# Optimization experiments

Measured on AMD Instinct MI355X. Metric: run time of the kernel, lower is better.

Reference implementation:

```python
import jax, jax.numpy as jnp
import numpy as np

B = 4096          # effective_batch_size (world_size=1)
D = 128           # embedding_dim
T = 0.5           # temperature
CW = 0.5          # confidence_weight
PT = 0.8          # positive_threshold (cosine)


def setup_inputs() -> dict:
    key = jax.random.key(0)
    emb = jax.random.normal(key, (B, D), dtype=jnp.float32)
    emb = emb / jnp.linalg.norm(emb, axis=1, keepdims=True)  # cosine-sim embeddings
    return {"embedding": emb}


def reference(embedding):
    b = embedding.shape[0]
    half = b // 2
    idx = jnp.arange(b)
    pos_idx = (idx + half) % b  # positive pair index (other augmented view)

    # exp(sim / T), [B, B]
    sim = jnp.exp(embedding @ embedding.T / T)

    # precomputed masks (world_size=1, rank=0, num_pos=2):
    # positive mask: the other view; negative mask: everything except self and its pair
    pos_mask = jnp.zeros((b, b), dtype=sim.dtype).at[idx, pos_idx].set(1.0)
    neg_mask = 1.0 - pos_mask - jnp.eye(b, dtype=sim.dtype)

    all_pos = sim * pos_mask
    all_neg = sim * neg_mask

    pos_sim = sim[idx, pos_idx]  # [B]

    # diff_sim: |sim - pos_sim| on upper triangle (j >= i), 3 elsewhere,
    # with diagonal and (i, i+half) for i < half also set to 3
    upper = idx[None, :] >= idx[:, None]
    excl = jnp.eye(b, dtype=bool) | ((idx[:, None] < half) & (idx[None, :] == idx[:, None] + half))
    diff_sim = jnp.where(upper & ~excl, jnp.abs(sim - pos_sim[:, None]), jnp.asarray(3.0, sim.dtype))

    # all argmin locations (torch.where(diff_sim == min)) -> boolean select mask
    min_mask = diff_sim == jnp.min(diff_sim)
    conf = (jnp.log(pos_sim) * T >= PT)[:, None]  # per-anchor confidence gate
    sel = min_mask & conf

    # false-negative reweighting (pos read of all_neg happens before neg update)
    new_pos = jnp.where(sel & (all_pos == 0.0), CW * all_neg, all_pos)
    new_neg = jnp.where(sel & (all_neg != 0.0), (1.0 - CW) * all_neg, all_neg)

    pos = jnp.sum(new_pos, axis=1)
    neg = jnp.sum(new_neg, axis=1)
    return -jnp.mean(jnp.log(pos / (pos + neg)))
```

## Files before the change

### kernel.cpp

```cpp
#include <hip/hip_runtime.h>
#include <hip/hip_bf16.h>
#include <math.h>

#define B_N  4096
#define HALF 2048
#define D_K  128
#define BT   128
#define NBT  32
#define NBLK (NBT * (NBT + 1) / 2)

typedef __attribute__((ext_vector_type(8))) short bf16x8;
typedef __attribute__((ext_vector_type(4))) float f32x4;

__device__ __forceinline__ void stage_tile_cvt(const float* __restrict__ emb,
                                               int row0, ushort* lds) {
    int t = threadIdx.x;
    const float4* src = (const float4*)(emb + (size_t)row0 * D_K);
    char* dst = (char*)lds;
#pragma unroll
    for (int it = 0; it < 8; ++it) {
        int f = t + 256 * it;
        int r = f >> 4;
        int c = f & 15;
        float4 v0 = src[r * 32 + c * 2];
        float4 v1 = src[r * 32 + c * 2 + 1];
        union { __hip_bfloat162 h; unsigned u; } c0, c1, c2, c3;
        c0.h = __float22bfloat162_rn(make_float2(v0.x, v0.y));
        c1.h = __float22bfloat162_rn(make_float2(v0.z, v0.w));
        c2.h = __float22bfloat162_rn(make_float2(v1.x, v1.y));
        c3.h = __float22bfloat162_rn(make_float2(v1.z, v1.w));
        uint4 w = {c0.u, c1.u, c2.u, c3.u};
        int byte = (r << 8) | (((c ^ (r & 7)) & 15) << 4);
        *(uint4*)(dst + byte) = w;
    }
}

__device__ __forceinline__ bf16x8 read_frag(const ushort* lds, int row, int kbyte) {
    int byte = ((row << 8) | kbyte) ^ ((row & 7) << 4);
    return *(const bf16x8*)((const char*)lds + byte);
}

__device__ __forceinline__ void tile_mfma_sw(const ushort* Al, const ushort* Bl,
                                             int lane, int wr, f32x4 acc[2][8]) {
#pragma unroll
    for (int m = 0; m < 2; ++m)
#pragma unroll
        for (int n = 0; n < 8; ++n) acc[m][n] = (f32x4){0.f, 0.f, 0.f, 0.f};

    int rA = wr * 32 + (lane & 15);
    int rB = (lane & 15);
    int kb0 = (lane >> 4) << 4;
#pragma unroll
    for (int ks = 0; ks < 4; ++ks) {
        int kb = ks * 64 + kb0;
        bf16x8 a[2], b[8];
#pragma unroll
        for (int m = 0; m < 2; ++m) a[m] = read_frag(Al, rA + m * 16, kb);
#pragma unroll
        for (int n = 0; n < 8; ++n) b[n] = read_frag(Bl, rB + n * 16, kb);
#pragma unroll
        for (int m = 0; m < 2; ++m)
#pragma unroll
            for (int n = 0; n < 8; ++n)
                acc[m][n] = __builtin_amdgcn_mfma_f32_16x16x32_bf16(
                    b[n], a[m], acc[m][n], 0, 0, 0);
    }
}

__global__ __launch_bounds__(256) void k0_prep(const float* __restrict__ emb,
                                               float* __restrict__ pos_sim,
                                               float* __restrict__ conf,
                                               float* __restrict__ neg_acc,
                                               unsigned* __restrict__ minbits,
                                               unsigned* __restrict__ counter) {
    int tid = threadIdx.x;
    int r   = blockIdx.x * 16 + (tid >> 4);
    int l16 = tid & 15;
    const float* a = emb + (size_t)r * D_K + l16 * 8;
    const float* b = emb + (size_t)(r ^ HALF) * D_K + l16 * 8;
    float4 x0 = *(const float4*)a,       x1 = *(const float4*)(a + 4);
    float4 y0 = *(const float4*)b,       y1 = *(const float4*)(b + 4);
    float d = 0.f;
    d = fmaf(x0.x, y0.x, d); d = fmaf(x0.y, y0.y, d);
    d = fmaf(x0.z, y0.z, d); d = fmaf(x0.w, y0.w, d);
    d = fmaf(x1.x, y1.x, d); d = fmaf(x1.y, y1.y, d);
    d = fmaf(x1.z, y1.z, d); d = fmaf(x1.w, y1.w, d);
#pragma unroll
    for (int off = 1; off < 16; off <<= 1) d += __shfl_xor(d, off);
    if (l16 == 0) {
        float ps = expf(d * 2.0f);
        pos_sim[r] = ps;
        conf[r]    = (logf(ps) * 0.5f >= 0.8f) ? 1.0f : 0.0f;
        neg_acc[r] = 0.f;
    }
    if (blockIdx.x == 0 && tid == 0) {
        *minbits = __float_as_uint(3.0f);
        *counter = 0u;
    }
}

__global__ __launch_bounds__(256, 2) void k1_main(const float* __restrict__ emb,
                                                  const float* __restrict__ pos_sim,
                                                  const float* __restrict__ conf,
                                                  float* __restrict__ neg_acc,
                                                  float* __restrict__ corrpart,
                                                  unsigned* __restrict__ block_min,
                                                  unsigned* __restrict__ minbits) {
    int t = blockIdx.x, bi = 0;
    while (t >= NBT - bi) { t -= NBT - bi; ++bi; }
    int bj = bi + t;
    bool diag = (bi == bj);
    bool post = (bj == (bi ^ 16));

    __shared__ ushort Al[BT * D_K];
    __shared__ ushort Bl[BT * D_K];
    stage_tile_cvt(emb, bi * BT, Al);
    if (!diag) stage_tile_cvt(emb, bj * BT, Bl);
    __syncthreads();
    const ushort* Bs = diag ? Al : Bl;

    int tid = threadIdx.x, lane = tid & 63, wr = tid >> 6;
    f32x4 acc[2][8];
    tile_mfma_sw(Al, Bs, lane, wr, acc);

#pragma unroll
    for (int m = 0; m < 2; ++m)
#pragma unroll
        for (int n = 0; n < 8; ++n)
#pragma unroll
            for (int reg = 0; reg < 4; ++reg)
                acc[m][n][reg] = __expf(acc[m][n][reg] * 2.0f);

    int ib = bi * BT + wr * 32 + (lane & 15);
    int jb = bj * BT + ((lane >> 4) << 2);

    float psi_[2];
    float lmin = 3.0f;
#pragma unroll
    for (int m = 0; m < 2; ++m) {
        int i = ib + m * 16;
        float psi = pos_sim[i];
        psi_[m] = psi;
        int pidx = i ^ HALF;
        float np0 = 0.f, np1 = 0.f, np2 = 0.f, np3 = 0.f;
        float l0 = 3.f, l1 = 3.f, l2 = 3.f, l3 = 3.f;
        if (!diag && !post) {
#pragma unroll
            for (int n = 0; n < 8; ++n) {
                float s0 = acc[m][n][0], s1 = acc[m][n][1];
                float s2 = acc[m][n][2], s3 = acc[m][n][3];
                np0 += s0; np1 += s1; np2 += s2; np3 += s3;
                l0 = fminf(l0, fabsf(s0 - psi)); l1 = fminf(l1, fabsf(s1 - psi));
                l2 = fminf(l2, fabsf(s2 - psi)); l3 = fminf(l3, fabsf(s3 - psi));
            }
        } else if (diag) {
#pragma unroll
            for (int n = 0; n < 8; ++n)
#pragma unroll
                for (int reg = 0; reg < 4; ++reg) {
                    float s = acc[m][n][reg];
                    int j = jb + n * 16 + reg;
                    if (j != i) np0 += s;
                    if (j > i)  l0 = fminf(l0, fabsf(s - psi));
                }
        } else {
#pragma unroll
            for (int n = 0; n < 8; ++n)
#pragma unroll
                for (int reg = 0; reg < 4; ++reg) {
                    float s = acc[m][n][reg];
                    int j = jb + n * 16 + reg;
                    if (j != pidx) {
                        np0 += s;
                        l0 = fminf(l0, fabsf(s - psi));
                    }
                }
        }
        float negp = (np0 + np1) + (np2 + np3);
        negp += __shfl_xor(negp, 16);
        negp += __shfl_xor(negp, 32);
        if (lane < 16) atomicAdd(&neg_acc[i], negp);
        lmin = fminf(lmin, fminf(fminf(l0, l1), fminf(l2, l3)));
    }

    if (!diag) {
        float colc[32];
#pragma unroll
        for (int n = 0; n < 8; ++n)
#pragma unroll
            for (int reg = 0; reg < 4; ++reg) {
                float s0 = acc[0][n][reg], s1 = acc[1][n][reg];
                if (post) {
                    int j = jb + n * 16 + reg;
                    if (j == (ib ^ HALF))        s0 = 0.f;
                    if (j == ((ib + 16) ^ HALF)) s1 = 0.f;
                }
                colc[n * 4 + reg] = s0 + s1;
            }
#pragma unroll
        for (int off = 1; off < 16; off <<= 1)
#pragma unroll
            for (int v = 0; v < 32; ++v)
                colc[v] += __shfl_xor(colc[v], off);
        if ((lane & 15) == 0) {
#pragma unroll
            for (int v = 0; v < 32; ++v)
                atomicAdd(&neg_acc[jb + (v >> 2) * 16 + (v & 3)], colc[v]);
        }
    }

#pragma unroll
    for (int off = 32; off; off >>= 1)
        lmin = fminf(lmin, __shfl_xor(lmin, off));
    __shared__ float wred[4];
    if (lane == 0) wred[wr] = lmin;
    __syncthreads();
    float bmin = fminf(fminf(wred[0], wred[1]), fminf(wred[2], wred[3]));
    if (tid == 0) {
        block_min[bi * NBT + bj] = __float_as_uint(bmin);
        atomicMin(minbits, __float_as_uint(bmin));
    }

    float corr_[2] = {0.f, 0.f};
    bool anyc = (conf[ib] != 0.f) || (conf[ib + 16] != 0.f);
    if (__any(anyc)) {
#pragma unroll
        for (int m = 0; m < 2; ++m) {
            int i = ib + m * 16;
            float psi = psi_[m];
            int pidx = i ^ HALF;
            bool ci = (conf[i] != 0.f);
            float corr = 0.f;
#pragma unroll
            for (int n = 0; n < 8; ++n)
#pragma unroll
                for (int reg = 0; reg < 4; ++reg) {
                    float s = acc[m][n][reg];
                    int j = jb + n * 16 + reg;
                    bool valid = diag ? (j > i) : (post ? (j != pidx) : true);
                    float d = valid ? fabsf(s - psi) : 3.0f;
                    if (ci && d == bmin) corr += 0.5f * s;
                }
            corr += __shfl_xor(corr, 16);
            corr += __shfl_xor(corr, 32);
            corr_[m] = corr;
        }
    }
    if (lane < 16) {
        corrpart[bj * B_N + ib]      = corr_[0];
        corrpart[bj * B_N + ib + 16] = corr_[1];
    }
}

__global__ __launch_bounds__(128) void k3_loss(const float* __restrict__ pos_sim,
                                               const float* __restrict__ neg_acc,
                                               const float* __restrict__ corrpart,
                                               const unsigned* __restrict__ block_min,
                                               const unsigned* __restrict__ minbits,
                                               float* __restrict__ partial,
                                               unsigned* __restrict__ counter,
                                               float* __restrict__ out) {
    int bi = blockIdx.x, t = threadIdx.x;
    int i = bi * 128 + t;
    unsigned gm = *minbits;
    float corr = 0.f;
    for (int bj = bi; bj < NBT; ++bj)
        if (block_min[bi * NBT + bj] == gm) corr += corrpart[bj * B_N + i];
    float neg = neg_acc[i] - corr;
    float pos = pos_sim[i] + corr;
    float l = logf(pos / (pos + neg));
#pragma unroll
    for (int off = 32; off; off >>= 1) l += __shfl_xor(l, off);
    __shared__ float w2[2];
    if ((t & 63) == 0) w2[t >> 6] = l;
    __syncthreads();
    if (t == 0) {
        partial[bi] = w2[0] + w2[1];
        __threadfence();
        unsigned c = atomicAdd((unsigned*)counter, 1u);
        if (c == NBT - 1) {
            __threadfence();
            float tot = 0.f;
            volatile float* vp = partial;
            for (int b = 0; b < NBT; ++b) tot += vp[b];
            *out = -tot / (float)B_N;
        }
    }
}

extern "C" void kernel_launch(void* const* d_in, const int* in_sizes, int n_in,
                              void* d_out, int out_size, void* d_ws, size_t ws_size,
                              hipStream_t stream) {
    const float* emb = (const float*)d_in[0];
    float* out = (float*)d_out;

    float* fbase = (float*)d_ws;
    float*    pos_sim   = fbase;
    float*    conf      = fbase + 4096;
    float*    neg_acc   = fbase + 8192;
    float*    corrpart  = fbase + 12288;
    float*    partial   = corrpart + NBT * B_N;
    unsigned* block_min = (unsigned*)(partial + 32);
    unsigned* minbits   = block_min + 1024;
    unsigned* counter   = minbits + 1;

    k0_prep<<<256, 256, 0, stream>>>(emb, pos_sim, conf, neg_acc, minbits, counter);
    k1_main<<<NBLK, 256, 0, stream>>>(emb, pos_sim, conf, neg_acc, corrpart,
                                      block_min, minbits);
    k3_loss<<<NBT, 128, 0, stream>>>(pos_sim, neg_acc, corrpart, block_min,
                                     minbits, partial, counter, out);
}
```

Baseline: 40.59 us.

## Precompute bf16 embeddings and stream full-row j-tiles with async LDS double buffering

```diff
diff --git a/kernel.cpp b/kernel.cpp
--- a/kernel.cpp
+++ b/kernel.cpp
@@ -5,34 +5,26 @@
 #define B_N  4096
 #define HALF 2048
 #define D_K  128
-#define BT   128
-#define NBT  32
-#define NBLK (NBT * (NBT + 1) / 2)
+#define TI   128
+#define TJ   64
+#define NTI  32
+#define NTJ  64
+#define JPB  4
+#define NJG  (NTJ / JPB)
 
 typedef __attribute__((ext_vector_type(8))) short bf16x8;
 typedef __attribute__((ext_vector_type(4))) float f32x4;
 
-__device__ __forceinline__ void stage_tile_cvt(const float* __restrict__ emb,
-                                               int row0, ushort* lds) {
-    int t = threadIdx.x;
-    const float4* src = (const float4*)(emb + (size_t)row0 * D_K);
-    char* dst = (char*)lds;
-#pragma unroll
-    for (int it = 0; it < 8; ++it) {
-        int f = t + 256 * it;
-        int r = f >> 4;
-        int c = f & 15;
-        float4 v0 = src[r * 32 + c * 2];
-        float4 v1 = src[r * 32 + c * 2 + 1];
-        union { __hip_bfloat162 h; unsigned u; } c0, c1, c2, c3;
-        c0.h = __float22bfloat162_rn(make_float2(v0.x, v0.y));
-        c1.h = __float22bfloat162_rn(make_float2(v0.z, v0.w));
-        c2.h = __float22bfloat162_rn(make_float2(v1.x, v1.y));
-        c3.h = __float22bfloat162_rn(make_float2(v1.z, v1.w));
-        uint4 w = {c0.u, c1.u, c2.u, c3.u};
-        int byte = (r << 8) | (((c ^ (r & 7)) & 15) << 4);
-        *(uint4*)(dst + byte) = w;
-    }
+__device__ __forceinline__ ushort f2bf(float x) {
+    unsigned u = __float_as_uint(x);
+    unsigned r = u + 0x7FFFu + ((u >> 16) & 1u);
+    return (ushort)(r >> 16);
+}
+
+__device__ __forceinline__ void gload_lds16(const ushort* g, ushort* l) {
+    __builtin_amdgcn_global_load_lds(
+        (const __attribute__((address_space(1))) unsigned int*)g,
+        (__attribute__((address_space(3))) unsigned int*)l, 16, 0, 0);
 }
 
 __device__ __forceinline__ bf16x8 read_frag(const ushort* lds, int row, int kbyte) {
@@ -40,234 +32,258 @@
     return *(const bf16x8*)((const char*)lds + byte);
 }
 
-__device__ __forceinline__ void tile_mfma_sw(const ushort* Al, const ushort* Bl,
-                                             int lane, int wr, f32x4 acc[2][8]) {
-#pragma unroll
-    for (int m = 0; m < 2; ++m)
-#pragma unroll
-        for (int n = 0; n < 8; ++n) acc[m][n] = (f32x4){0.f, 0.f, 0.f, 0.f};
-
-    int rA = wr * 32 + (lane & 15);
-    int rB = (lane & 15);
-    int kb0 = (lane >> 4) << 4;
-#pragma unroll
-    for (int ks = 0; ks < 4; ++ks) {
-        int kb = ks * 64 + kb0;
-        bf16x8 a[2], b[8];
-#pragma unroll
-        for (int m = 0; m < 2; ++m) a[m] = read_frag(Al, rA + m * 16, kb);
-#pragma unroll
-        for (int n = 0; n < 8; ++n) b[n] = read_frag(Bl, rB + n * 16, kb);
-#pragma unroll
-        for (int m = 0; m < 2; ++m)
-#pragma unroll
-            for (int n = 0; n < 8; ++n)
-                acc[m][n] = __builtin_amdgcn_mfma_f32_16x16x32_bf16(
-                    b[n], a[m], acc[m][n], 0, 0, 0);
-    }
-}
-
 __global__ __launch_bounds__(256) void k0_prep(const float* __restrict__ emb,
+                                               ushort* __restrict__ embh,
                                                float* __restrict__ pos_sim,
                                                float* __restrict__ conf,
                                                float* __restrict__ neg_acc,
-                                               unsigned* __restrict__ minbits,
+                                               float* __restrict__ corrpart,
                                                unsigned* __restrict__ counter) {
     int tid = threadIdx.x;
-    int r   = blockIdx.x * 16 + (tid >> 4);
-    int l16 = tid & 15;
-    const float* a = emb + (size_t)r * D_K + l16 * 8;
-    const float* b = emb + (size_t)(r ^ HALF) * D_K + l16 * 8;
-    float4 x0 = *(const float4*)a,       x1 = *(const float4*)(a + 4);
-    float4 y0 = *(const float4*)b,       y1 = *(const float4*)(b + 4);
-    float d = 0.f;
-    d = fmaf(x0.x, y0.x, d); d = fmaf(x0.y, y0.y, d);
-    d = fmaf(x0.z, y0.z, d); d = fmaf(x0.w, y0.w, d);
-    d = fmaf(x1.x, y1.x, d); d = fmaf(x1.y, y1.y, d);
-    d = fmaf(x1.z, y1.z, d); d = fmaf(x1.w, y1.w, d);
-#pragma unroll
-    for (int off = 1; off < 16; off <<= 1) d += __shfl_xor(d, off);
-    if (l16 == 0) {
-        float ps = expf(d * 2.0f);
-        pos_sim[r] = ps;
-        conf[r]    = (logf(ps) * 0.5f >= 0.8f) ? 1.0f : 0.0f;
-        neg_acc[r] = 0.f;
-    }
-    if (blockIdx.x == 0 && tid == 0) {
-        *minbits = __float_as_uint(3.0f);
-        *counter = 0u;
-    }
-}
-
-__global__ __launch_bounds__(256, 2) void k1_main(const float* __restrict__ emb,
+    int gtid = blockIdx.x * 256 + tid;
+    float4 v = ((const float4*)emb)[gtid];
+    ushort4 h;
+    h.x = f2bf(v.x); h.y = f2bf(v.y); h.z = f2bf(v.z); h.w = f2bf(v.w);
+    ((ushort4*)embh)[gtid] = h;
+    ((float2*)corrpart)[gtid] = make_float2(0.f, 0.f);
+
+    if (blockIdx.x < 256) {
+        int r   = blockIdx.x * 16 + (tid >> 4);
+        int l16 = tid & 15;
+        const float* a = emb + (size_t)r * D_K + l16 * 8;
+        const float* b = emb + (size_t)(r ^ HALF) * D_K + l16 * 8;
+        float4 x0 = *(const float4*)a, x1 = *(const float4*)(a + 4);
+        float4 y0 = *(const float4*)b, y1 = *(const float4*)(b + 4);
+        float d = 0.f;
+        d = fmaf(x0.x, y0.x, d); d = fmaf(x0.y, y0.y, d);
+        d = fmaf(x0.z, y0.z, d); d = fmaf(x0.w, y0.w, d);
+        d = fmaf(x1.x, y1.x, d); d = fmaf(x1.y, y1.y, d);
+        d = fmaf(x1.z, y1.z, d); d = fmaf(x1.w, y1.w, d);
+#pragma unroll
+        for (int off = 1; off < 16; off <<= 1) d += __shfl_xor(d, off);
+        if (l16 == 0) {
+            float ps = expf(d * 2.0f);
+            pos_sim[r] = ps;
+            conf[r]    = (logf(ps) * 0.5f >= 0.8f) ? 1.0f : 0.0f;
+            neg_acc[r] = 0.f;
+        }
+    }
+    if (gtid == 0) *counter = 0u;
+}
+
+__global__ __launch_bounds__(256, 2) void k1_main(const ushort* __restrict__ embh,
                                                   const float* __restrict__ pos_sim,
                                                   const float* __restrict__ conf,
                                                   float* __restrict__ neg_acc,
                                                   float* __restrict__ corrpart,
-                                                  unsigned* __restrict__ block_min,
-                                                  unsigned* __restrict__ minbits) {
-    int t = blockIdx.x, bi = 0;
-    while (t >= NBT - bi) { t -= NBT - bi; ++bi; }
-    int bj = bi + t;
-    bool diag = (bi == bj);
-    bool post = (bj == (bi ^ 16));
-
-    __shared__ ushort Al[BT * D_K];
-    __shared__ ushort Bl[BT * D_K];
-    stage_tile_cvt(emb, bi * BT, Al);
-    if (!diag) stage_tile_cvt(emb, bj * BT, Bl);
+                                                  unsigned* __restrict__ tile_min) {
+    int bi = blockIdx.y, jg = blockIdx.x;
+    __shared__ ushort Al[TI * D_K];
+    __shared__ ushort B0[TJ * D_K];
+    __shared__ ushort B1[TJ * D_K];
+
+    int tid = threadIdx.x, lane = tid & 63, wr = tid >> 6;
+    int l15 = lane & 15;
+
+    {
+        const ushort* srcA = embh + (size_t)bi * TI * D_K;
+#pragma unroll
+        for (int it = 0; it < 8; ++it) {
+            int f = tid + 256 * it;
+            int r = f >> 4, c = f & 15;
+            int g = (r << 4) | (c ^ (r & 7));
+            gload_lds16(srcA + g * 8, Al + f * 8);
+        }
+        const ushort* srcB = embh + (size_t)(jg * JPB) * TJ * D_K;
+#pragma unroll
+        for (int it = 0; it < 4; ++it) {
+            int f = tid + 256 * it;
+            int r = f >> 4, c = f & 15;
+            int g = (r << 4) | (c ^ (r & 7));
+            gload_lds16(srcB + g * 8, B0 + f * 8);
+        }
+    }
+
+    int I0  = bi * TI + wr * 32;
+    int jtd = I0 >> 6;
+    float psi0 = pos_sim[I0 + l15];
+    float psi1 = pos_sim[I0 + 16 + l15];
+    float cf0  = conf[I0 + l15];
+    float cf1  = conf[I0 + 16 + l15];
+    bool anyc  = __any((cf0 != 0.f) || (cf1 != 0.f));
+    float negacc0 = 0.f, negacc1 = 0.f;
+
     __syncthreads();
-    const ushort* Bs = diag ? Al : Bl;
-
-    int tid = threadIdx.x, lane = tid & 63, wr = tid >> 6;
-    f32x4 acc[2][8];
-    tile_mfma_sw(Al, Bs, lane, wr, acc);
-
-#pragma unroll
-    for (int m = 0; m < 2; ++m)
-#pragma unroll
-        for (int n = 0; n < 8; ++n)
-#pragma unroll
-            for (int reg = 0; reg < 4; ++reg)
-                acc[m][n][reg] = __expf(acc[m][n][reg] * 2.0f);
-
-    int ib = bi * BT + wr * 32 + (lane & 15);
-    int jb = bj * BT + ((lane >> 4) << 2);
-
-    float psi_[2];
-    float lmin = 3.0f;
-#pragma unroll
-    for (int m = 0; m < 2; ++m) {
-        int i = ib + m * 16;
-        float psi = pos_sim[i];
-        psi_[m] = psi;
-        int pidx = i ^ HALF;
-        float np0 = 0.f, np1 = 0.f, np2 = 0.f, np3 = 0.f;
-        float l0 = 3.f, l1 = 3.f, l2 = 3.f, l3 = 3.f;
-        if (!diag && !post) {
-#pragma unroll
-            for (int n = 0; n < 8; ++n) {
-                float s0 = acc[m][n][0], s1 = acc[m][n][1];
-                float s2 = acc[m][n][2], s3 = acc[m][n][3];
-                np0 += s0; np1 += s1; np2 += s2; np3 += s3;
-                l0 = fminf(l0, fabsf(s0 - psi)); l1 = fminf(l1, fabsf(s1 - psi));
-                l2 = fminf(l2, fabsf(s2 - psi)); l3 = fminf(l3, fabsf(s3 - psi));
+
+    int rA  = wr * 32 + l15;
+    int rB  = l15;
+    int kb0 = (lane >> 4) << 4;
+    int jr4 = (lane >> 4) << 2;
+
+#pragma unroll
+    for (int t = 0; t < JPB; ++t) {
+        const ushort* Bc = (t & 1) ? B1 : B0;
+        ushort*       Bn = (t & 1) ? B0 : B1;
+        int jt = jg * JPB + t;
+
+        if (t + 1 < JPB) {
+            const ushort* srcB = embh + (size_t)(jt + 1) * TJ * D_K;
+#pragma unroll
+            for (int it = 0; it < 4; ++it) {
+                int f = tid + 256 * it;
+                int r = f >> 4, c = f & 15;
+                int g = (r << 4) | (c ^ (r & 7));
+                gload_lds16(srcB + g * 8, Bn + f * 8);
             }
-        } else if (diag) {
-#pragma unroll
-            for (int n = 0; n < 8; ++n)
-#pragma unroll
-                for (int reg = 0; reg < 4; ++reg) {
-                    float s = acc[m][n][reg];
-                    int j = jb + n * 16 + reg;
-                    if (j != i) np0 += s;
-                    if (j > i)  l0 = fminf(l0, fabsf(s - psi));
-                }
-        } else {
-#pragma unroll
-            for (int n = 0; n < 8; ++n)
-#pragma unroll
-                for (int reg = 0; reg < 4; ++reg) {
-                    float s = acc[m][n][reg];
-                    int j = jb + n * 16 + reg;
-                    if (j != pidx) {
-                        np0 += s;
-                        l0 = fminf(l0, fabsf(s - psi));
+        }
+
+        f32x4 acc[2][4];
+#pragma unroll
+        for (int m = 0; m < 2; ++m)
+#pragma unroll
+            for (int n = 0; n < 4; ++n) acc[m][n] = (f32x4){0.f, 0.f, 0.f, 0.f};
+#pragma unroll
+        for (int ks = 0; ks < 4; ++ks) {
+            int kb = ks * 64 + kb0;
+            bf16x8 a0 = read_frag(Al, rA, kb);
+            bf16x8 a1 = read_frag(Al, rA + 16, kb);
+            bf16x8 b[4];
+#pragma unroll
+            for (int n = 0; n < 4; ++n) b[n] = read_frag(Bc, rB + n * 16, kb);
+#pragma unroll
+            for (int n = 0; n < 4; ++n) {
+                acc[0][n] = __builtin_amdgcn_mfma_f32_16x16x32_bf16(b[n], a0, acc[0][n], 0, 0, 0);
+                acc[1][n] = __builtin_amdgcn_mfma_f32_16x16x32_bf16(b[n], a1, acc[1][n], 0, 0, 0);
+            }
+        }
+#pragma unroll
+        for (int m = 0; m < 2; ++m)
+#pragma unroll
+            for (int n = 0; n < 4; ++n)
+#pragma unroll
+                for (int reg = 0; reg < 4; ++reg)
+                    acc[m][n][reg] = __expf(acc[m][n][reg] * 2.0f);
+
+        int j0 = jt * TJ;
+        bool mixed = (jt == jtd), postt = (jt == (jtd ^ 32)), upT = (jt > jtd);
+        float tmin = 3.0f;
+#pragma unroll
+        for (int m = 0; m < 2; ++m) {
+            int i = I0 + m * 16 + l15;
+            float psi = m ? psi1 : psi0;
+            float np = 0.f;
+            if (mixed) {
+#pragma unroll
+                for (int n = 0; n < 4; ++n)
+#pragma unroll
+                    for (int reg = 0; reg < 4; ++reg) {
+                        float s = acc[m][n][reg];
+                        int j = j0 + n * 16 + jr4 + reg;
+                        if (j != i) np += s;
+                        if (j > i)  tmin = fminf(tmin, fabsf(s - psi));
+                    }
+            } else if (postt) {
+                int pidx = i ^ HALF;
+#pragma unroll
+                for (int n = 0; n < 4; ++n)
+#pragma unroll
+                    for (int reg = 0; reg < 4; ++reg) {
+                        float s = acc[m][n][reg];
+                        int j = j0 + n * 16 + jr4 + reg;
+                        if (j != pidx) {
+                            np += s;
+                            if (upT) tmin = fminf(tmin, fabsf(s - psi));
+                        }
+                    }
+            } else {
+                float l0 = 3.f, l1 = 3.f, l2 = 3.f, l3 = 3.f;
+#pragma unroll
+                for (int n = 0; n < 4; ++n) {
+                    float s0 = acc[m][n][0], s1 = acc[m][n][1];
+                    float s2 = acc[m][n][2], s3 = acc[m][n][3];
+                    np += (s0 + s1) + (s2 + s3);
+                    if (upT) {
+                        l0 = fminf(l0, fabsf(s0 - psi)); l1 = fminf(l1, fabsf(s1 - psi));
+                        l2 = fminf(l2, fabsf(s2 - psi)); l3 = fminf(l3, fabsf(s3 - psi));
                     }
                 }
-        }
-        float negp = (np0 + np1) + (np2 + np3);
-        negp += __shfl_xor(negp, 16);
-        negp += __shfl_xor(negp, 32);
-        if (lane < 16) atomicAdd(&neg_acc[i], negp);
-        lmin = fminf(lmin, fminf(fminf(l0, l1), fminf(l2, l3)));
-    }
-
-    if (!diag) {
-        float colc[32];
-#pragma unroll
-        for (int n = 0; n < 8; ++n)
-#pragma unroll
-            for (int reg = 0; reg < 4; ++reg) {
-                float s0 = acc[0][n][reg], s1 = acc[1][n][reg];
-                if (post) {
-                    int j = jb + n * 16 + reg;
-                    if (j == (ib ^ HALF))        s0 = 0.f;
-                    if (j == ((ib + 16) ^ HALF)) s1 = 0.f;
-                }
-                colc[n * 4 + reg] = s0 + s1;
+                tmin = fminf(tmin, fminf(fminf(l0, l1), fminf(l2, l3)));
             }
-#pragma unroll
-        for (int off = 1; off < 16; off <<= 1)
-#pragma unroll
-            for (int v = 0; v < 32; ++v)
-                colc[v] += __shfl_xor(colc[v], off);
-        if ((lane & 15) == 0) {
-#pragma unroll
-            for (int v = 0; v < 32; ++v)
-                atomicAdd(&neg_acc[jb + (v >> 2) * 16 + (v & 3)], colc[v]);
-        }
-    }
-
-#pragma unroll
-    for (int off = 32; off; off >>= 1)
-        lmin = fminf(lmin, __shfl_xor(lmin, off));
-    __shared__ float wred[4];
-    if (lane == 0) wred[wr] = lmin;
-    __syncthreads();
-    float bmin = fminf(fminf(wred[0], wred[1]), fminf(wred[2], wred[3]));
-    if (tid == 0) {
-        block_min[bi * NBT + bj] = __float_as_uint(bmin);
-        atomicMin(minbits, __float_as_uint(bmin));
-    }
-
-    float corr_[2] = {0.f, 0.f};
-    bool anyc = (conf[ib] != 0.f) || (conf[ib + 16] != 0.f);
-    if (__any(anyc)) {
-#pragma unroll
-        for (int m = 0; m < 2; ++m) {
-            int i = ib + m * 16;
-            float psi = psi_[m];
-            int pidx = i ^ HALF;
-            bool ci = (conf[i] != 0.f);
-            float corr = 0.f;
-#pragma unroll
-            for (int n = 0; n < 8; ++n)
-#pragma unroll
-                for (int reg = 0; reg < 4; ++reg) {
-                    float s = acc[m][n][reg];
-                    int j = jb + n * 16 + reg;
-                    bool valid = diag ? (j > i) : (post ? (j != pidx) : true);
-                    float d = valid ? fabsf(s - psi) : 3.0f;
-                    if (ci && d == bmin) corr += 0.5f * s;
-                }
-            corr += __shfl_xor(corr, 16);
-            corr += __shfl_xor(corr, 32);
-            corr_[m] = corr;
-        }
-    }
+            if (m) negacc1 += np; else negacc0 += np;
+        }
+#pragma unroll
+        for (int off = 32; off; off >>= 1)
+            tmin = fminf(tmin, __shfl_xor(tmin, off));
+        if (lane == 0)
+            tile_min[(bi * 4 + wr) * NTJ + jt] = __float_as_uint(tmin);
+
+        if (anyc) {
+#pragma unroll
+            for (int m = 0; m < 2; ++m) {
+                int i = I0 + m * 16 + l15;
+                float psi = m ? psi1 : psi0;
+                bool ci = ((m ? cf1 : cf0) != 0.f);
+                float corr = 0.f;
+#pragma unroll
+                for (int n = 0; n < 4; ++n)
+#pragma unroll
+                    for (int reg = 0; reg < 4; ++reg) {
+                        float s = acc[m][n][reg];
+                        int j = j0 + n * 16 + jr4 + reg;
+                        float d = 3.0f;
+                        if (mixed)      { if (j > i) d = fabsf(s - psi); }
+                        else if (postt) { if (upT && j != (i ^ HALF)) d = fabsf(s - psi); }
+                        else if (upT)   d = fabsf(s - psi);
+                        if (ci && d == tmin) corr += 0.5f * s;
+                    }
+                corr += __shfl_xor(corr, 16);
+                corr += __shfl_xor(corr, 32);
+                if (lane < 16) corrpart[(size_t)jt * B_N + i] = corr;
+            }
+        }
+        __syncthreads();
+    }
+
+    negacc0 += __shfl_xor(negacc0, 16);
+    negacc0 += __shfl_xor(negacc0, 32);
+    negacc1 += __shfl_xor(negacc1, 16);
+    negacc1 += __shfl_xor(negacc1, 32);
     if (lane < 16) {
-        corrpart[bj * B_N + ib]      = corr_[0];
-        corrpart[bj * B_N + ib + 16] = corr_[1];
+        atomicAdd(&neg_acc[I0 + lane],      negacc0);
+        atomicAdd(&neg_acc[I0 + 16 + lane], negacc1);
     }
 }
 
 __global__ __launch_bounds__(128) void k3_loss(const float* __restrict__ pos_sim,
                                                const float* __restrict__ neg_acc,
                                                const float* __restrict__ corrpart,
-                                               const unsigned* __restrict__ block_min,
-                                               const unsigned* __restrict__ minbits,
+                                               const unsigned* __restrict__ tile_min,
                                                float* __restrict__ partial,
                                                unsigned* __restrict__ counter,
                                                float* __restrict__ out) {
-    int bi = blockIdx.x, t = threadIdx.x;
+    int t = threadIdx.x, bi = blockIdx.x;
+    unsigned gmv = 0xFFFFFFFFu;
+#pragma unroll
+    for (int k = 0; k < 64; ++k) gmv = min(gmv, tile_min[t + 128 * k]);
+#pragma unroll
+    for (int off = 32; off; off >>= 1) {
+        unsigned o = (unsigned)__shfl_xor((int)gmv, off);
+        gmv = min(gmv, o);
+    }
+    __shared__ unsigned gred[2];
+    if ((t & 63) == 0) gred[t >> 6] = gmv;
+    __syncthreads();
+    unsigned gm = min(gred[0], gred[1]);
+
     int i = bi * 128 + t;
-    unsigned gm = *minbits;
+    int si = i >> 5;
     float corr = 0.f;
-    for (int bj = bi; bj < NBT; ++bj)
-        if (block_min[bi * NBT + bj] == gm) corr += corrpart[bj * B_N + i];
+#pragma unroll 8
+    for (int jt = 0; jt < NTJ; ++jt)
+        if (tile_min[si * NTJ + jt] == gm)
+            corr += corrpart[(size_t)jt * B_N + i];
+    float pos = pos_sim[i] + corr;
     float neg = neg_acc[i] - corr;
-    float pos = pos_sim[i] + corr;
     float l = logf(pos / (pos + neg));
 #pragma unroll
     for (int off = 32; off; off >>= 1) l += __shfl_xor(l, off);
@@ -277,12 +293,12 @@
     if (t == 0) {
         partial[bi] = w2[0] + w2[1];
         __threadfence();
-        unsigned c = atomicAdd((unsigned*)counter, 1u);
-        if (c == NBT - 1) {
+        unsigned c = atomicAdd(counter, 1u);
+        if (c == NTI - 1) {
             __threadfence();
             float tot = 0.f;
             volatile float* vp = partial;
-            for (int b = 0; b < NBT; ++b) tot += vp[b];
+            for (int b = 0; b < NTI; ++b) tot += vp[b];
             *out = -tot / (float)B_N;
         }
     }
@@ -294,19 +310,21 @@
     const float* emb = (const float*)d_in[0];
     float* out = (float*)d_out;
 
-    float* fbase = (float*)d_ws;
+    char* ws = (char*)d_ws;
+    ushort*   embh      = (ushort*)ws;
+    float*    fbase     = (float*)(ws + 1048576);
     float*    pos_sim   = fbase;
     float*    conf      = fbase + 4096;
     float*    neg_acc   = fbase + 8192;
     float*    corrpart  = fbase + 12288;
-    float*    partial   = corrpart + NBT * B_N;
-    unsigned* block_min = (unsigned*)(partial + 32);
-    unsigned* minbits   = block_min + 1024;
-    unsigned* counter   = minbits + 1;
-
-    k0_prep<<<256, 256, 0, stream>>>(emb, pos_sim, conf, neg_acc, minbits, counter);
-    k1_main<<<NBLK, 256, 0, stream>>>(emb, pos_sim, conf, neg_acc, corrpart,
-                                      block_min, minbits);
-    k3_loss<<<NBT, 128, 0, stream>>>(pos_sim, neg_acc, corrpart, block_min,
-                                     minbits, partial, counter, out);
-}
+    float*    partial   = corrpart + (size_t)NTJ * B_N;
+    unsigned* tile_min  = (unsigned*)(partial + 32);
+    unsigned* counter   = tile_min + 128 * NTJ;
+
+    k0_prep<<<512, 256, 0, stream>>>(emb, embh, pos_sim, conf, neg_acc,
+                                     corrpart, counter);
+    k1_main<<<dim3(NJG, NTI), 256, 0, stream>>>(embh, pos_sim, conf, neg_acc,
+                                                corrpart, tile_min);
+    k3_loss<<<NTI, 128, 0, stream>>>(pos_sim, neg_acc, corrpart, tile_min,
+                                     partial, counter, out);
+}
```

Result: faster. 32.72 us (-19.4%).
